# Kernel tuning notes

Hardware: AMD Instinct MI355X
Metric: run time of the kernel (lower is better)

## Reference

```python
import jax, jax.numpy as jnp
import numpy as np
from jax import lax

B, S, T = 64, 512, 48
E_WORD, E_FLAG, E_PIN = 200, 50, 50
E = E_WORD + E_FLAG + E_PIN  # 300
H = 256  # hidden_dim // 2 per direction
V_WORD, V_FLAG, V_PIN = 20000, 64, 500
NEG = -10000.0


def setup_inputs() -> dict:
    key = jax.random.key(0)
    ks = jax.random.split(key, 20)
    sc = 0.05
    return {
        "word_ids": jax.random.randint(ks[0], (B, S), 0, V_WORD),
        "flag_ids": jax.random.randint(ks[1], (B, S), 0, V_FLAG),
        "pinyin_ids": jax.random.randint(ks[2], (B, S), 0, V_PIN),
        "emb_word": jax.random.normal(ks[3], (V_WORD, E_WORD), jnp.float32),
        "emb_flag": jax.random.normal(ks[4], (V_FLAG, E_FLAG), jnp.float32),
        "emb_pinyin": jax.random.normal(ks[5], (V_PIN, E_PIN), jnp.float32),
        "Wih_f": jax.random.normal(ks[6], (4 * H, E), jnp.float32) * sc,
        "Whh_f": jax.random.normal(ks[7], (4 * H, H), jnp.float32) * sc,
        "bih_f": jnp.zeros((4 * H,), jnp.float32),
        "bhh_f": jnp.zeros((4 * H,), jnp.float32),
        "Wih_b": jax.random.normal(ks[8], (4 * H, E), jnp.float32) * sc,
        "Whh_b": jax.random.normal(ks[9], (4 * H, H), jnp.float32) * sc,
        "bih_b": jnp.zeros((4 * H,), jnp.float32),
        "bhh_b": jnp.zeros((4 * H,), jnp.float32),
        "h0": jax.random.normal(ks[10], (2, B, H), jnp.float32),
        "c0": jax.random.normal(ks[11], (2, B, H), jnp.float32),
        "W_out": jax.random.normal(ks[12], (T, 2 * H), jnp.float32) * sc,
        "b_out": jnp.zeros((T,), jnp.float32),
        "transitions": jax.random.normal(ks[13], (T, T), jnp.float32),
    }


def _run_lstm(x_sbe, Wih, Whh, bih, bhh, h0, c0, reverse):
    # x_sbe: [S, B, E]; torch LSTM gate order i, f, g, o
    xs = x_sbe[::-1] if reverse else x_sbe
    gx = jnp.einsum('sbe,ge->sbg', xs, Wih) + bih + bhh  # [S, B, 4H]

    def step(carry, g_t):
        h, c = carry
        g = g_t + h @ Whh.T
        i, f, gg, o = jnp.split(g, 4, axis=-1)
        c = jax.nn.sigmoid(f) * c + jax.nn.sigmoid(i) * jnp.tanh(gg)
        h = jax.nn.sigmoid(o) * jnp.tanh(c)
        return (h, c), h

    _, hs = lax.scan(step, (h0, c0), gx)  # hs: [S, B, H]
    return hs[::-1] if reverse else hs


def reference(word_ids, flag_ids, pinyin_ids, emb_word, emb_flag, emb_pinyin,
              Wih_f, Whh_f, bih_f, bhh_f, Wih_b, Whh_b, bih_b, bhh_b,
              h0, c0, W_out, b_out, transitions):
    # _embed_concat: per-feature embedding lookup, concat on feature dim
    embeds = jnp.concatenate([
        emb_word[word_ids], emb_flag[flag_ids], emb_pinyin[pinyin_ids]
    ], axis=-1)  # [B, S, E]

    x = embeds.transpose(1, 0, 2)  # [S, B, E]
    hs_f = _run_lstm(x, Wih_f, Whh_f, bih_f, bhh_f, h0[0], c0[0], False)
    hs_b = _run_lstm(x, Wih_b, Whh_b, bih_b, bhh_b, h0[1], c0[1], True)
    lstm_out = jnp.concatenate([hs_f, hs_b], axis=-1)  # [S, B, 2H]
    feats = jnp.einsum('sbh,th->sbt', lstm_out, W_out) + b_out  # [S, B, T]

    # Viterbi decode, vectorized over tags and batch, sequential over time
    init_vvars = jnp.full((B, T), NEG, jnp.float32)

    def vstep(fv, feat_t):
        # scores[b, next, prev] = fv[b, prev] + transitions[next, prev]
        scores = fv[:, None, :] + transitions[None, :, :]
        bp = jnp.argmax(scores, axis=-1)  # [B, T]
        fv_new = jnp.max(scores, axis=-1) + feat_t
        return fv_new, bp

    terminal, bptrs = lax.scan(vstep, init_vvars, feats)  # bptrs: [S, B, T]

    last_tag = jnp.argmax(terminal, axis=-1)  # [B]
    path_score = jnp.max(terminal, axis=-1)   # [B]

    def back_step(tag, bp_t):
        prev = jnp.take_along_axis(bp_t, tag[:, None], axis=1)[:, 0]
        return prev, prev

    _, prevs = lax.scan(back_step, last_tag, bptrs[::-1])  # [S, B]
    # best_path reversed + pop(start): drop the earliest backpointer
    best_path = jnp.concatenate([prevs[::-1][1:], last_tag[None]], axis=0).T  # [B, S]
    return path_score, best_path
```

## Files before the change

### kernel.cpp

```cpp
#include <hip/hip_runtime.h>
#include <hip/hip_bf16.h>
#include <hip/hip_fp16.h>
#include <math.h>

#define BB 64
#define SS 512
#define TT 48
#define EE 300
#define EP 320
#define HH 256
#define G4 1024
#define NG 2048
#define NEGV -10000.0f
#define SWQ (0.30f / 127.0f)

#define NWV 65536
#define NWL 65536

#define DPP0(x, ctrl) __builtin_amdgcn_update_dpp(0, (int)(x), (ctrl), 0xf, 0xf, false)

typedef _Float16 f16x8 __attribute__((ext_vector_type(8)));
typedef float f32x4 __attribute__((ext_vector_type(4)));

__device__ __forceinline__ float sigf(float x) { return 1.0f / (1.0f + __expf(-x)); }
__device__ __forceinline__ float tanhf_(float x) {
    float e = __expf(2.0f * x);
    return 1.0f - 2.0f / (e + 1.0f);
}

__device__ __forceinline__ int dot4(unsigned int h, unsigned int w, int acc) {
#if __has_builtin(__builtin_amdgcn_sdot4)
    return __builtin_amdgcn_sdot4((int)h, (int)w, acc, false);
#else
    acc += (int)(signed char)(h)       * (int)(signed char)(w);
    acc += (int)(signed char)(h >> 8)  * (int)(signed char)(w >> 8);
    acc += (int)(signed char)(h >> 16) * (int)(signed char)(w >> 16);
    acc += (int)(signed char)(h >> 24) * (int)(signed char)(w >> 24);
    return acc;
#endif
}

__device__ __forceinline__ float dot2u(unsigned int h, unsigned int w, float acc) {
#if __has_builtin(__builtin_amdgcn_fdot2)
    typedef _Float16 h2v __attribute__((ext_vector_type(2)));
    union { unsigned int u; h2v v; } H, W;
    H.u = h; W.u = w;
    return __builtin_amdgcn_fdot2(H.v, W.v, acc, false);
#else
    __half2 hh = *(__half2*)&h, ww = *(__half2*)&w;
    float2 hf = __half22float2(hh), wf = __half22float2(ww);
    return acc + hf.x * wf.x + hf.y * wf.y;
#endif
}

__device__ __forceinline__ unsigned int packh2(float lo, float hi) {
    union { __half2 h; unsigned int u; } p;
    p.h = __floats2half2_rn(lo, hi);
    return p.u;
}

__device__ __forceinline__ unsigned int q8(float x) {
    int q = __float2int_rn(fminf(fmaxf(x, -127.0f), 127.0f));
    return (unsigned int)(q & 0xff);
}

__global__ __launch_bounds__(256) void k_prep(
    const float* __restrict__ Whh_f, const float* __restrict__ Whh_b,
    const float* __restrict__ Wih_f, const float* __restrict__ Wih_b,
    const float* __restrict__ bih_f, const float* __restrict__ bhh_f,
    const float* __restrict__ bih_b, const float* __restrict__ bhh_b,
    const float* __restrict__ W_out,
    __half* __restrict__ WIHT2, float* __restrict__ BIAS,
    unsigned int* __restrict__ WV8, unsigned int* __restrict__ WL8,
    unsigned int* __restrict__ WOTP2)
{
    int i = blockIdx.x * 256 + threadIdx.x;
    const int NWIHT2 = NG * EP;
    if (i < NWIHT2) {
        int n = i / EP, k = i % EP;
        int d = n >> 10, c = n & 1023;
        int row = (c & 3) * 256 + (c >> 2);
        const float* w = d ? Wih_b : Wih_f;
        WIHT2[i] = __float2half(k < EE ? w[row * EE + k] : 0.0f);
        return;
    }
    i -= NWIHT2;
    if (i < NG) {
        int d = i >> 10, c = i & 1023;
        int row = (c & 3) * 256 + (c >> 2);
        BIAS[i] = d ? (bih_b[row] + bhh_b[row]) : (bih_f[row] + bhh_f[row]);
        return;
    }
    i -= NG;
    if (i < NWV) {
        int d = i >> 15, rem = i & 32767;
        int p = rem >> 9, t = rem & 511;
        int G = t >> 3, r = t & 7;
        int lc = p >> 3, kq = p & 7;
        int col = 16 * G + lc;
        int row = (col & 3) * 256 + (col >> 2);
        int k0 = 32 * r + 4 * kq;
        const float* W = d ? Whh_b : Whh_f;
        unsigned int v = 0;
        #pragma unroll
        for (int bb = 0; bb < 4; bb++)
            v |= q8(W[row * HH + k0 + bb] * (1.0f / SWQ)) << (8 * bb);
        WV8[i] = v;
        return;
    }
    i -= NWV;
    if (i < NWL) {
        int d = i >> 15, rem = i & 32767;
        int g = rem >> 11, i3 = rem & 2047;
        int t = i3 >> 2, m = i3 & 3;
        int G = t >> 3, r = t & 7;
        int lc = 8 + (g >> 1), kq = (g & 1) * 4 + m;
        int col = 16 * G + lc;
        int row = (col & 3) * 256 + (col >> 2);
        int k0 = 32 * r + 4 * kq;
        const float* W = d ? Whh_b : Whh_f;
        unsigned int v = 0;
        #pragma unroll
        for (int bb = 0; bb < 4; bb++)
            v |= q8(W[row * HH + k0 + bb] * (1.0f / SWQ)) << (8 * bb);
        WL8[i] = v;
        return;
    }
    i -= NWL;
    if (i < 48 * 256) {
        int u4 = i >> 2;
        int kp4 = u4 / 48, t = u4 % 48;
        int kp = kp4 * 4 + (i & 3);
        WOTP2[i] = packh2(W_out[t * 512 + 2 * kp], W_out[t * 512 + 2 * kp + 1]);
        return;
    }
}

__global__ __launch_bounds__(320) void k_embed(
    const int* __restrict__ wid, const int* __restrict__ fid, const int* __restrict__ pid,
    const float* __restrict__ ew, const float* __restrict__ ef, const float* __restrict__ ep,
    __half* __restrict__ X)
{
    int t = threadIdx.x;
    int sb0 = blockIdx.x * 16;
    #pragma unroll 4
    for (int it = 0; it < 16; it++) {
        int sb = sb0 + it;
        int s = sb >> 6, b = sb & 63;
        int w = wid[b * SS + s];
        int f = fid[b * SS + s];
        int p = pid[b * SS + s];
        float v;
        if (t < 200)      v = ew[w * 200 + t];
        else if (t < 250) v = ef[f * 50 + (t - 200)];
        else if (t < 300) v = ep[p * 50 + (t - 250)];
        else              v = 0.0f;
        X[(size_t)sb * EP + t] = __float2half(v);
    }
}

__global__ __launch_bounds__(256) void k_gemm(
    const __half* __restrict__ X, const __half* __restrict__ WT,
    const float* __restrict__ BIAS, __half* __restrict__ GX)
{
    int tid = threadIdx.x;
    int l = tid & 63, wn = tid >> 6;
    int m0 = blockIdx.y * 64, nb = blockIdx.x * 256 + wn * 64;
    int lr = l & 15, lg = l >> 4;

    f32x4 acc[16];
    #pragma unroll
    for (int i = 0; i < 16; i++) acc[i] = (f32x4){0.0f, 0.0f, 0.0f, 0.0f};

    const __half* ab = X  + (size_t)(m0 + lr) * EP + lg * 8;
    const __half* bb = WT + (size_t)(nb + lr) * EP + lg * 8;
    for (int kc = 0; kc < 10; kc++) {
        f16x8 af[4], bf[4];
        #pragma unroll
        for (int mi = 0; mi < 4; mi++)
            af[mi] = *(const f16x8*)(ab + (size_t)mi * 16 * EP + kc * 32);
        #pragma unroll
        for (int nj = 0; nj < 4; nj++)
            bf[nj] = *(const f16x8*)(bb + (size_t)nj * 16 * EP + kc * 32);
        #pragma unroll
        for (int mi = 0; mi < 4; mi++)
            #pragma unroll
            for (int nj = 0; nj < 4; nj++)
                acc[mi * 4 + nj] = __builtin_amdgcn_mfma_f32_16x16x32_f16(
                    af[mi], bf[nj], acc[mi * 4 + nj], 0, 0, 0);
    }
    #pragma unroll
    for (int nj = 0; nj < 4; nj++) {
        float bias = BIAS[nb + nj * 16 + lr];
        #pragma unroll
        for (int mi = 0; mi < 4; mi++) {
            f32x4 a = acc[mi * 4 + nj];
            #pragma unroll
            for (int v = 0; v < 4; v++) {
                int m = m0 + mi * 16 + lg * 4 + v;
                GX[(size_t)m * NG + nb + nj * 16 + lr] = __float2half(a[v] + bias);
            }
        }
    }
}

__global__ __launch_bounds__(512, 1) void k_lstm(
    const unsigned int* __restrict__ WV8, const uint4* __restrict__ WL8,
    const __half* __restrict__ GX, const float* __restrict__ h0,
    const float* __restrict__ c0, __half* __restrict__ HS)
{
    __shared__ uint4 LW[16 * 512];
    __shared__ unsigned int h8[2][64];
    int wg = blockIdx.x; int dir = wg >> 6, b = wg & 63;
    int t = threadIdx.x;
    int G = t >> 3, r = t & 7, rp = r & 3;

    const uint4* wl = WL8 + (size_t)dir * (16 * 512);
    #pragma unroll
    for (int g = 0; g < 16; g++) LW[g * 512 + t] = wl[g * 512 + t];

    const unsigned int* wv = WV8 + (size_t)dir * (64 * 512);
    unsigned int WR[64];
    #pragma unroll
    for (int p = 0; p < 64; p++) {
        unsigned int tmp = wv[p * 512 + t];
        asm volatile("v_mov_b32 %0, %1" : "=v"(WR[p]) : "v"(tmp));
    }

    size_t sbase = (size_t)dir * BB * HH + b * HH;
    float c = c0[sbase + 4 * G + rp];
    if (t < 64) {
        unsigned int v = 0;
        #pragma unroll
        for (int u = 0; u < 4; u++)
            v |= q8(h0[sbase + 4 * t + u] * (127.0f / 5.0f)) << (8 * u);
        h8[0][t] = v;
    }
    __syncthreads();

    const __half* gxbase = GX + (dir << 10);
    int s0 = dir ? (SS - 1) : 0;
    int unit = 4 * G + rp;
    uint2 gx = *(const uint2*)(gxbase + (size_t)(s0 * BB + b) * NG + 4 * unit);

    int cur = 0;
    for (int tt = 0; tt < SS; tt++) {
        int s  = dir ? (SS - 1 - tt) : tt;
        int tn = (tt + 1 < SS) ? (tt + 1) : tt;
        int sn = dir ? (SS - 1 - tn) : tn;
        uint2 gx_n = *(const uint2*)(gxbase + (size_t)(sn * BB + b) * NG + 4 * unit);

        uint4 hA = *(const uint4*)&h8[cur][8 * r];
        uint4 hB = *(const uint4*)&h8[cur][8 * r + 4];
        unsigned int hr[8] = { hA.x, hA.y, hA.z, hA.w, hB.x, hB.y, hB.z, hB.w };

        int acc[16];
        #pragma unroll
        for (int m = 0; m < 16; m++) acc[m] = 0;
        #pragma unroll
        for (int p = 0; p < 64; p++)
            acc[p >> 3] = dot4(hr[p & 7], WR[p], acc[p >> 3]);
        #pragma unroll
        for (int g = 0; g < 16; g++) {
            uint4 w = LW[g * 512 + t];
            const int lc = 8 + (g >> 1), kq0 = (g & 1) * 4;
            acc[lc] = dot4(hr[kq0 + 0], w.x, acc[lc]);
            acc[lc] = dot4(hr[kq0 + 1], w.y, acc[lc]);
            acc[lc] = dot4(hr[kq0 + 2], w.z, acc[lc]);
            acc[lc] = dot4(hr[kq0 + 3], w.w, acc[lc]);
        }

        #pragma unroll
        for (int m = 0; m < 16; m++) acc[m] += DPP0(acc[m], 0x141);
        bool keep2 = (r & 2) == 0;
        int b8v[8];
        #pragma unroll
        for (int m = 0; m < 8; m++) {
            int send = keep2 ? acc[8 + m] : acc[m];
            int got  = DPP0(send, 0x4E);
            b8v[m] = (keep2 ? acc[m] : acc[8 + m]) + got;
        }
        bool keep1 = (r & 1) == 0;
        int f4v[4];
        #pragma unroll
        for (int m = 0; m < 4; m++) {
            int send = keep1 ? b8v[4 + m] : b8v[m];
            int got  = DPP0(send, 0xB1);
            f4v[m] = (keep1 ? b8v[m] : b8v[4 + m]) + got;
        }

        float st = SWQ * ((tt == 0) ? (5.0f / 127.0f) : (1.0f / 127.0f));
        __half2 g01 = *(__half2*)&gx.x;  float2 f01 = __half22float2(g01);
        __half2 g23 = *(__half2*)&gx.y;  float2 f23 = __half22float2(g23);
        float pi = f01.x + st * (float)f4v[0];
        float pf = f01.y + st * (float)f4v[1];
        float pg = f23.x + st * (float)f4v[2];
        float po = f23.y + st * (float)f4v[3];
        c = sigf(pf) * c + sigf(pi) * tanhf_(pg);
        float h = sigf(po) * tanhf_(c);

        unsigned int hv = q8(h * 127.0f) << (8 * rp);
        hv |= (unsigned int)DPP0(hv, 0xB1);
        hv |= (unsigned int)DPP0(hv, 0x4E);
        if (r == 0) h8[cur ^ 1][G] = hv;

        float hnx = __int_as_float(DPP0(__float_as_int(h), 0x39));
        if (r == 0 || r == 2)
            *(unsigned int*)(HS + (size_t)(s * BB + b) * 512 + (dir << 8) + 4 * G + r)
                = packh2(h, hnx);

        __syncthreads();
        cur ^= 1;
        gx = gx_n;
    }
}

__global__ __launch_bounds__(384) void k_feats(
    const unsigned int* __restrict__ HSU, const uint4* __restrict__ W2,
    const float* __restrict__ b_out, float* __restrict__ F)
{
    __shared__ unsigned int rl_u[8 * 256];
    int sb0 = blockIdx.x * 8;
    int tid = threadIdx.x;
    for (int i = tid; i < 512; i += 384) {
        int row = i >> 6, u4c = i & 63;
        uint4 v = *(const uint4*)(HSU + (size_t)(sb0 + row) * 256 + u4c * 4);
        *(uint4*)&rl_u[row * 256 + u4c * 4] = v;
    }
    __syncthreads();
    int rr = tid / TT, t = tid % TT;
    float acc = b_out[t];
    #pragma unroll 8
    for (int kp4 = 0; kp4 < 64; kp4++) {
        uint4 ru = *(const uint4*)&rl_u[rr * 256 + kp4 * 4];
        uint4 wu = W2[kp4 * 48 + t];
        acc = dot2u(ru.x, wu.x, acc);
        acc = dot2u(ru.y, wu.y, acc);
        acc = dot2u(ru.z, wu.z, acc);
        acc = dot2u(ru.w, wu.w, acc);
    }
    F[(size_t)(sb0 + rr) * TT + t] = acc;
}

__global__ __launch_bounds__(64) void k_viterbi(
    const float* __restrict__ F, const float* __restrict__ trans,
    float* __restrict__ out)
{
    int b = blockIdx.x;
    int tid = threadIdx.x;
    __shared__ float tl[TT * TT];
    __shared__ float fv[TT];
    __shared__ unsigned char bp[SS * TT];
    __shared__ unsigned char path[SS];
    for (int i = tid; i < TT * TT; i += 64) {
        int prev = i / TT, nx = i % TT;
        tl[i] = trans[nx * TT + prev];
    }
    if (tid < TT) fv[tid] = NEGV;
    float fcur = (tid < TT) ? F[(size_t)(0 * BB + b) * TT + tid] : 0.0f;
    for (int s = 0; s < SS; s++) {
        float fnext = (tid < TT && s + 1 < SS)
                    ? F[(size_t)((s + 1) * BB + b) * TT + tid] : 0.0f;
        if (tid < TT) {
            float best = -1e30f; int bi = 0;
            #pragma unroll 8
            for (int prev = 0; prev < TT; prev++) {
                float sc = fv[prev] + tl[prev * TT + tid];
                if (sc > best) { best = sc; bi = prev; }
            }
            bp[s * TT + tid] = (unsigned char)bi;
            fv[tid] = best + fcur;
        }
        fcur = fnext;
    }
    if (tid == 0) {
        float best = fv[0]; int bi = 0;
        for (int i = 1; i < TT; i++) if (fv[i] > best) { best = fv[i]; bi = i; }
        out[b] = best;
        int tag = bi;
        path[SS - 1] = (unsigned char)tag;
        for (int jj = SS - 2; jj >= 0; jj--) {
            tag = bp[(jj + 1) * TT + tag];
            path[jj] = (unsigned char)tag;
        }
    }
    for (int jj = tid; jj < SS; jj += 64)
        out[BB + (size_t)b * SS + jj] = (float)path[jj];
}

extern "C" void kernel_launch(void* const* d_in, const int* in_sizes, int n_in,
                              void* d_out, int out_size, void* d_ws, size_t ws_size,
                              hipStream_t stream) {
    const int*   wid    = (const int*)d_in[0];
    const int*   fid    = (const int*)d_in[1];
    const int*   pid    = (const int*)d_in[2];
    const float* ew     = (const float*)d_in[3];
    const float* ef     = (const float*)d_in[4];
    const float* epn    = (const float*)d_in[5];
    const float* Wih_f  = (const float*)d_in[6];
    const float* Whh_f  = (const float*)d_in[7];
    const float* bih_f  = (const float*)d_in[8];
    const float* bhh_f  = (const float*)d_in[9];
    const float* Wih_b  = (const float*)d_in[10];
    const float* Whh_b  = (const float*)d_in[11];
    const float* bih_b  = (const float*)d_in[12];
    const float* bhh_b  = (const float*)d_in[13];
    const float* h0     = (const float*)d_in[14];
    const float* c0     = (const float*)d_in[15];
    const float* W_out  = (const float*)d_in[16];
    const float* b_out  = (const float*)d_in[17];
    const float* trans  = (const float*)d_in[18];

    char* p = (char*)d_ws;
    auto alloc = [&](size_t bytes) { char* r = p; p += (bytes + 255) & ~(size_t)255; return r; };
    __half*       X      = (__half*)alloc((size_t)32768 * EP * 2);
    __half*       GX     = (__half*)alloc((size_t)32768 * NG * 2);
    __half*       HS     = (__half*)alloc((size_t)32768 * 512 * 2);
    unsigned int* WV8    = (unsigned int*)alloc((size_t)NWV * 4);
    unsigned int* WL8    = (unsigned int*)alloc((size_t)NWL * 4);
    __half*       WIHT2  = (__half*)alloc((size_t)NG * EP * 2);
    float*        BIAS   = (float*)alloc((size_t)NG * 4);
    unsigned int* WOTP2  = (unsigned int*)alloc((size_t)48 * 256 * 4);
    float*        F      = (float*)alloc((size_t)32768 * TT * 4);

    k_prep<<<3128, 256, 0, stream>>>(Whh_f, Whh_b, Wih_f, Wih_b,
                                     bih_f, bhh_f, bih_b, bhh_b, W_out,
                                     WIHT2, BIAS, WV8, WL8, WOTP2);
    k_embed<<<2048, 320, 0, stream>>>(wid, fid, pid, ew, ef, epn, X);
    k_gemm<<<dim3(8, 512), 256, 0, stream>>>(X, WIHT2, BIAS, GX);
    k_lstm<<<128, 512, 0, stream>>>(WV8, (const uint4*)WL8, GX, h0, c0, HS);
    k_feats<<<4096, 384, 0, stream>>>((const unsigned int*)HS, (const uint4*)WOTP2, b_out, F);
    k_viterbi<<<64, 64, 0, stream>>>(F, trans, (float*)d_out);
}
```

Measured before the change: 1.464 ms.

## Fuse prep and embed kernels; split Viterbi max over four thread groups

```diff
diff --git a/kernel.cpp b/kernel.cpp
--- a/kernel.cpp
+++ b/kernel.cpp
@@ -64,7 +64,8 @@
     return (unsigned int)(q & 0xff);
 }
 
-__global__ __launch_bounds__(256) void k_prep(
+#define PREP_BLOCKS 2503
+__global__ __launch_bounds__(320) void k_pe(
     const float* __restrict__ Whh_f, const float* __restrict__ Whh_b,
     const float* __restrict__ Wih_f, const float* __restrict__ Wih_b,
     const float* __restrict__ bih_f, const float* __restrict__ bhh_f,
@@ -72,9 +73,32 @@
     const float* __restrict__ W_out,
     __half* __restrict__ WIHT2, float* __restrict__ BIAS,
     unsigned int* __restrict__ WV8, unsigned int* __restrict__ WL8,
-    unsigned int* __restrict__ WOTP2)
+    unsigned int* __restrict__ WOTP2,
+    const int* __restrict__ wid, const int* __restrict__ fid,
+    const int* __restrict__ pid,
+    const float* __restrict__ ew, const float* __restrict__ ef,
+    const float* __restrict__ ep, __half* __restrict__ X)
 {
-    int i = blockIdx.x * 256 + threadIdx.x;
+    if (blockIdx.x >= PREP_BLOCKS) {
+        int t = threadIdx.x;
+        int sb0 = (blockIdx.x - PREP_BLOCKS) * 16;
+        #pragma unroll 4
+        for (int it = 0; it < 16; it++) {
+            int sb = sb0 + it;
+            int s = sb >> 6, b = sb & 63;
+            int w = wid[b * SS + s];
+            int f = fid[b * SS + s];
+            int p = pid[b * SS + s];
+            float v;
+            if (t < 200)      v = ew[w * 200 + t];
+            else if (t < 250) v = ef[f * 50 + (t - 200)];
+            else if (t < 300) v = ep[p * 50 + (t - 250)];
+            else              v = 0.0f;
+            X[(size_t)sb * EP + t] = __float2half(v);
+        }
+        return;
+    }
+    int i = blockIdx.x * 320 + threadIdx.x;
     const int NWIHT2 = NG * EP;
     if (i < NWIHT2) {
         int n = i / EP, k = i % EP;
@@ -136,29 +160,6 @@
     }
 }
 
-__global__ __launch_bounds__(320) void k_embed(
-    const int* __restrict__ wid, const int* __restrict__ fid, const int* __restrict__ pid,
-    const float* __restrict__ ew, const float* __restrict__ ef, const float* __restrict__ ep,
-    __half* __restrict__ X)
-{
-    int t = threadIdx.x;
-    int sb0 = blockIdx.x * 16;
-    #pragma unroll 4
-    for (int it = 0; it < 16; it++) {
-        int sb = sb0 + it;
-        int s = sb >> 6, b = sb & 63;
-        int w = wid[b * SS + s];
-        int f = fid[b * SS + s];
-        int p = pid[b * SS + s];
-        float v;
-        if (t < 200)      v = ew[w * 200 + t];
-        else if (t < 250) v = ef[f * 50 + (t - 200)];
-        else if (t < 300) v = ep[p * 50 + (t - 250)];
-        else              v = 0.0f;
-        X[(size_t)sb * EP + t] = __float2half(v);
-    }
-}
-
 __global__ __launch_bounds__(256) void k_gemm(
     const __half* __restrict__ X, const __half* __restrict__ WT,
     const float* __restrict__ BIAS, __half* __restrict__ GX)
@@ -342,36 +343,67 @@
     F[(size_t)(sb0 + rr) * TT + t] = acc;
 }
 
-__global__ __launch_bounds__(64) void k_viterbi(
+__global__ __launch_bounds__(256) void k_viterbi(
     const float* __restrict__ F, const float* __restrict__ trans,
     float* __restrict__ out)
 {
     int b = blockIdx.x;
     int tid = threadIdx.x;
-    __shared__ float tl[TT * TT];
-    __shared__ float fv[TT];
+    int nx = tid % TT, pc = tid / TT;
+    __shared__ __align__(16) float fv[TT];
+    __shared__ float red[4][TT];
+    __shared__ unsigned char redi[4][TT];
     __shared__ unsigned char bp[SS * TT];
     __shared__ unsigned char path[SS];
-    for (int i = tid; i < TT * TT; i += 64) {
-        int prev = i / TT, nx = i % TT;
-        tl[i] = trans[nx * TT + prev];
+
+    float treg[12];
+    if (pc < 4) {
+        int p0 = pc * 12;
+        float4 t0 = *(const float4*)(trans + nx * TT + p0);
+        float4 t1 = *(const float4*)(trans + nx * TT + p0 + 4);
+        float4 t2 = *(const float4*)(trans + nx * TT + p0 + 8);
+        treg[0] = t0.x; treg[1]  = t0.y; treg[2]  = t0.z; treg[3]  = t0.w;
+        treg[4] = t1.x; treg[5]  = t1.y; treg[6]  = t1.z; treg[7]  = t1.w;
+        treg[8] = t2.x; treg[9]  = t2.y; treg[10] = t2.z; treg[11] = t2.w;
     }
     if (tid < TT) fv[tid] = NEGV;
-    float fcur = (tid < TT) ? F[(size_t)(0 * BB + b) * TT + tid] : 0.0f;
+    __syncthreads();
+
+    float f0 = (tid < TT) ? F[(size_t)(0 * BB + b) * TT + tid] : 0.0f;
+    float f1 = (tid < TT) ? F[(size_t)(1 * BB + b) * TT + tid] : 0.0f;
     for (int s = 0; s < SS; s++) {
-        float fnext = (tid < TT && s + 1 < SS)
-                    ? F[(size_t)((s + 1) * BB + b) * TT + tid] : 0.0f;
+        float f2 = (tid < TT && s + 2 < SS)
+                 ? F[(size_t)((s + 2) * BB + b) * TT + tid] : 0.0f;
+        if (pc < 4) {
+            int p0 = pc * 12;
+            float4 v0 = *(const float4*)&fv[p0];
+            float4 v1 = *(const float4*)&fv[p0 + 4];
+            float4 v2 = *(const float4*)&fv[p0 + 8];
+            float fvv[12] = { v0.x, v0.y, v0.z, v0.w,
+                              v1.x, v1.y, v1.z, v1.w,
+                              v2.x, v2.y, v2.z, v2.w };
+            float best = -1e30f; int bi = 0;
+            #pragma unroll
+            for (int k = 0; k < 12; k++) {
+                float sc = fvv[k] + treg[k];
+                if (sc > best) { best = sc; bi = p0 + k; }
+            }
+            red[pc][nx] = best;
+            redi[pc][nx] = (unsigned char)bi;
+        }
+        __syncthreads();
         if (tid < TT) {
-            float best = -1e30f; int bi = 0;
-            #pragma unroll 8
-            for (int prev = 0; prev < TT; prev++) {
-                float sc = fv[prev] + tl[prev * TT + tid];
-                if (sc > best) { best = sc; bi = prev; }
+            float best = red[0][tid]; int bi = redi[0][tid];
+            #pragma unroll
+            for (int q = 1; q < 4; q++) {
+                float v = red[q][tid];
+                if (v > best) { best = v; bi = redi[q][tid]; }
             }
             bp[s * TT + tid] = (unsigned char)bi;
-            fv[tid] = best + fcur;
-        }
-        fcur = fnext;
+            fv[tid] = best + f0;
+        }
+        __syncthreads();
+        f0 = f1; f1 = f2;
     }
     if (tid == 0) {
         float best = fv[0]; int bi = 0;
@@ -384,7 +416,8 @@
             path[jj] = (unsigned char)tag;
         }
     }
-    for (int jj = tid; jj < SS; jj += 64)
+    __syncthreads();
+    for (int jj = tid; jj < SS; jj += 256)
         out[BB + (size_t)b * SS + jj] = (float)path[jj];
 }
 
@@ -423,12 +456,12 @@
     unsigned int* WOTP2  = (unsigned int*)alloc((size_t)48 * 256 * 4);
     float*        F      = (float*)alloc((size_t)32768 * TT * 4);
 
-    k_prep<<<3128, 256, 0, stream>>>(Whh_f, Whh_b, Wih_f, Wih_b,
-                                     bih_f, bhh_f, bih_b, bhh_b, W_out,
-                                     WIHT2, BIAS, WV8, WL8, WOTP2);
-    k_embed<<<2048, 320, 0, stream>>>(wid, fid, pid, ew, ef, epn, X);
+    k_pe<<<PREP_BLOCKS + 2048, 320, 0, stream>>>(
+        Whh_f, Whh_b, Wih_f, Wih_b, bih_f, bhh_f, bih_b, bhh_b, W_out,
+        WIHT2, BIAS, WV8, WL8, WOTP2,
+        wid, fid, pid, ew, ef, epn, X);
     k_gemm<<<dim3(8, 512), 256, 0, stream>>>(X, WIHT2, BIAS, GX);
     k_lstm<<<128, 512, 0, stream>>>(WV8, (const uint4*)WL8, GX, h0, c0, HS);
     k_feats<<<4096, 384, 0, stream>>>((const unsigned int*)HS, (const uint4*)WOTP2, b_out, F);
-    k_viterbi<<<64, 64, 0, stream>>>(F, trans, (float*)d_out);
-}
+    k_viterbi<<<64, 256, 0, stream>>>(F, trans, (float*)d_out);
+}
```

New measurement: 1.179 ms. -19.4%, faster.
